# Performance work log

Measured on AMD Instinct MI355X. Metric: run time of the kernel, lower is better.

The kernel has to match this reference:

```python
import jax, jax.numpy as jnp
import numpy as np

B, C, L = 16, 256, 4096
P, Q = 100, 20


def setup_inputs() -> dict:
    key = jax.random.key(0)
    k1, k2, k3, k4 = jax.random.split(key, 4)
    X = jax.random.normal(k1, (B, C, L), dtype=jnp.float32)
    projections = jax.random.normal(k2, (P, C), dtype=jnp.float32)
    # min < max per projection. Projected values ~ N(0, sqrt(C)), so scale ~ sqrt(C).
    scale = jnp.sqrt(jnp.float32(C))
    min_vals = -scale * (1.0 + jax.random.uniform(k3, (P,), dtype=jnp.float32))
    max_vals = scale * (1.0 + jax.random.uniform(k4, (P,), dtype=jnp.float32))
    return {"X": X, "projections": projections, "min_vals": min_vals, "max_vals": max_vals}


def reference(X, projections, min_vals, max_vals):
    # conv1d with kernel size 1 == per-position projection: [B,C,L] x [P,C] -> [B,P,L]
    a = jnp.einsum('bcl,pc->bpl', X, projections)
    # all quantile thresholds at once: thr[p,q] = min + (max-min)*(q+1)/(Q+1)
    fracs = (jnp.arange(1, Q + 1, dtype=jnp.float32)) / jnp.float32(Q + 1)  # [Q]
    thr = min_vals[:, None] + (max_vals - min_vals)[:, None] * fracs[None, :]  # [P,Q]
    # set[b,p,l,q] = a[b,p,l] < thr[p,q]
    set_ = (a[:, :, :, None] < thr[None, :, None, :]).astype(jnp.float32)  # [B,P,L,Q]
    cdf = jnp.mean(set_, axis=2)  # [B,P,Q]
    # transpose(2,1) -> [B,L,P,Q]; reshape -> [B,L,P*Q]; transpose(2,1) -> [B,P*Q,L]
    set_out = jnp.transpose(set_, (0, 2, 1, 3)).reshape(B, L, P * Q)
    set_out = jnp.transpose(set_out, (0, 2, 1))  # [B, P*Q, L]
    cdf_out = cdf.reshape(B, P * Q)
    return (cdf_out, set_out)
```

## Files before the change

kernel.cpp:

```cpp
#include <hip/hip_runtime.h>

#define Bsz 16
#define Cc  256
#define Ll  4096
#define Pp  100
#define Qq  20
#define PQ  (Pp * Qq)

#define LTILE 1024
#define NLT   (Ll / LTILE)
#define GP    10
#define NPG   (Pp / GP)

typedef float f32x4 __attribute__((ext_vector_type(4)));

__global__ __launch_bounds__(256) void csf_main(
    const float* __restrict__ X,
    const float* __restrict__ proj,
    const float* __restrict__ mn,
    const float* __restrict__ mx,
    float* __restrict__ cdf,
    float* __restrict__ set_out) {
    const int lt  = blockIdx.x;
    const int pg  = blockIdx.y;
    const int b   = blockIdx.z;
    const int tid = threadIdx.x;
    const int l0  = lt * LTILE + tid * 4;
    const int p0  = __builtin_amdgcn_readfirstlane(pg * GP);

    const float* Xb = X + (size_t)b * Cc * Ll + l0;

    float acc[GP][4];
#pragma unroll
    for (int i = 0; i < GP; i++)
#pragma unroll
        for (int k = 0; k < 4; k++) acc[i][k] = 0.0f;

#pragma unroll 4
    for (int c = 0; c < Cc; c++) {
        const f32x4 x = *(const f32x4*)(Xb + (size_t)c * Ll);
#pragma unroll
        for (int i = 0; i < GP; i++) {
            const float w = proj[(size_t)(p0 + i) * Cc + c];
            acc[i][0] = __builtin_fmaf(x.x, w, acc[i][0]);
            acc[i][1] = __builtin_fmaf(x.y, w, acc[i][1]);
            acc[i][2] = __builtin_fmaf(x.z, w, acc[i][2]);
            acc[i][3] = __builtin_fmaf(x.w, w, acc[i][3]);
        }
    }

    float fr[Qq];
#pragma unroll
    for (int q = 0; q < Qq; q++) fr[q] = __fdiv_rn((float)(q + 1), 21.0f);

    float* ob = set_out + (size_t)b * PQ * Ll + l0;
    const bool lane0 = ((tid & 63) == 0);

#pragma unroll 1
    for (int i = 0; i < GP; i++) {
        const int p = p0 + i;
        const float mnp = mn[p];
        const float mxp = mx[p];
        const float d = __fsub_rn(mxp, mnp);
#pragma unroll
        for (int q = 0; q < Qq; q++) {
            const float thr = __fadd_rn(mnp, __fmul_rn(d, fr[q]));
            const bool b0 = acc[i][0] < thr;
            const bool b1 = acc[i][1] < thr;
            const bool b2 = acc[i][2] < thr;
            const bool b3 = acc[i][3] < thr;
            f32x4 o;
            o.x = b0 ? 1.0f : 0.0f;
            o.y = b1 ? 1.0f : 0.0f;
            o.z = b2 ? 1.0f : 0.0f;
            o.w = b3 ? 1.0f : 0.0f;
            __builtin_nontemporal_store(o, (f32x4*)(ob + (size_t)(p * Qq + q) * Ll));
            const int cnt = __popcll(__ballot(b0)) + __popcll(__ballot(b1))
                          + __popcll(__ballot(b2)) + __popcll(__ballot(b3));
            if (lane0) {
                atomicAdd(&cdf[(size_t)b * PQ + p * Qq + q],
                          (float)cnt * (1.0f / (float)Ll));
            }
        }
    }
}

extern "C" void kernel_launch(void* const* d_in, const int* in_sizes, int n_in,
                              void* d_out, int out_size, void* d_ws, size_t ws_size,
                              hipStream_t stream) {
    const float* X    = (const float*)d_in[0];
    const float* proj = (const float*)d_in[1];
    const float* mn   = (const float*)d_in[2];
    const float* mx   = (const float*)d_in[3];

    float* cdf     = (float*)d_out;
    float* set_out = cdf + (size_t)Bsz * PQ;

    (void)hipMemsetAsync(cdf, 0, (size_t)Bsz * PQ * sizeof(float), stream);

    dim3 grid(NLT, NPG, Bsz);
    csf_main<<<grid, 256, 0, stream>>>(X, proj, mn, mx, cdf, set_out);
}
```

Measured before the change: 603.1 us.

## Split into projection kernel plus threshold-expansion kernel via workspace buffer

```diff
diff --git a/kernel.cpp b/kernel.cpp
--- a/kernel.cpp
+++ b/kernel.cpp
@@ -7,14 +7,109 @@
 #define Qq  20
 #define PQ  (Pp * Qq)
 
-#define LTILE 1024
-#define NLT   (Ll / LTILE)
-#define GP    10
-#define NPG   (Pp / GP)
-
 typedef float f32x4 __attribute__((ext_vector_type(4)));
 
-__global__ __launch_bounds__(256) void csf_main(
+
+#define K1_PPB 25
+__global__ __launch_bounds__(256) void csf_proj(
+    const float* __restrict__ X,
+    const float* __restrict__ proj,
+    float* __restrict__ a_out) {
+    const int lt = blockIdx.x;
+    const int pg = blockIdx.y;
+    const int b  = blockIdx.z;
+    const int tid  = threadIdx.x;
+    const int wv   = tid >> 6;
+    const int lane = tid & 63;
+    const int l0   = lt * 1024 + wv * 256 + lane * 4;
+    const int p0   = __builtin_amdgcn_readfirstlane(pg * K1_PPB);
+
+    const float* Xb = X + (size_t)b * Cc * Ll + l0;
+    const float* pj = proj + (size_t)p0 * Cc;
+
+    float acc[K1_PPB][4];
+#pragma unroll
+    for (int i = 0; i < K1_PPB; i++)
+#pragma unroll
+        for (int k = 0; k < 4; k++) acc[i][k] = 0.0f;
+
+#pragma unroll 8
+    for (int c = 0; c < Cc; c++) {
+        const f32x4 x = *(const f32x4*)(Xb + (size_t)c * Ll);
+#pragma unroll
+        for (int i = 0; i < K1_PPB; i++) {
+            const float w = pj[(size_t)i * Cc + c];
+            acc[i][0] = __builtin_fmaf(x.x, w, acc[i][0]);
+            acc[i][1] = __builtin_fmaf(x.y, w, acc[i][1]);
+            acc[i][2] = __builtin_fmaf(x.z, w, acc[i][2]);
+            acc[i][3] = __builtin_fmaf(x.w, w, acc[i][3]);
+        }
+    }
+
+    float* ao = a_out + ((size_t)b * Pp + p0) * Ll + l0;
+#pragma unroll
+    for (int i = 0; i < K1_PPB; i++) {
+        f32x4 v;
+        v.x = acc[i][0]; v.y = acc[i][1]; v.z = acc[i][2]; v.w = acc[i][3];
+        *(f32x4*)(ao + (size_t)i * Ll) = v;
+    }
+}
+
+__global__ __launch_bounds__(256) void csf_expand(
+    const float* __restrict__ a_in,
+    const float* __restrict__ mn,
+    const float* __restrict__ mx,
+    float* __restrict__ cdf,
+    float* __restrict__ set_out) {
+    const int p = blockIdx.x;
+    const int b = blockIdx.y;
+    const int tid  = threadIdx.x;
+    const int wv   = tid >> 6;
+    const int lane = tid & 63;
+
+    const float* ar = a_in + ((size_t)b * Pp + p) * Ll + wv * 1024 + lane * 4;
+    f32x4 av[4];
+#pragma unroll
+    for (int k = 0; k < 4; k++) av[k] = *(const f32x4*)(ar + k * 256);
+
+    const float mnp = mn[p];
+    const float mxp = mx[p];
+    const float d = __fsub_rn(mxp, mnp);
+
+    float* ob = set_out + ((size_t)b * PQ + (size_t)p * Qq) * Ll
+              + wv * 1024 + lane * 4;
+    const bool lane0 = (lane == 0);
+
+#pragma unroll 1
+    for (int q = 0; q < Qq; q++) {
+        const float fr  = __fdiv_rn((float)(q + 1), 21.0f);
+        const float thr = __fadd_rn(mnp, __fmul_rn(d, fr));
+        float* orow = ob + (size_t)q * Ll;
+        int cnt = 0;
+#pragma unroll
+        for (int k = 0; k < 4; k++) {
+            const bool b0 = av[k].x < thr;
+            const bool b1 = av[k].y < thr;
+            const bool b2 = av[k].z < thr;
+            const bool b3 = av[k].w < thr;
+            f32x4 o;
+            o.x = b0 ? 1.0f : 0.0f;
+            o.y = b1 ? 1.0f : 0.0f;
+            o.z = b2 ? 1.0f : 0.0f;
+            o.w = b3 ? 1.0f : 0.0f;
+            *(f32x4*)(orow + k * 256) = o;
+            cnt += __popcll(__ballot(b0)) + __popcll(__ballot(b1))
+                 + __popcll(__ballot(b2)) + __popcll(__ballot(b3));
+        }
+        if (lane0) {
+            atomicAdd(&cdf[(size_t)b * PQ + p * Qq + q],
+                      (float)cnt * (1.0f / (float)Ll));
+        }
+    }
+}
+
+#define FGP 10
+__global__ __launch_bounds__(256) void csf_fused(
     const float* __restrict__ X,
     const float* __restrict__ proj,
     const float* __restrict__ mn,
@@ -25,22 +120,20 @@
     const int pg  = blockIdx.y;
     const int b   = blockIdx.z;
     const int tid = threadIdx.x;
-    const int l0  = lt * LTILE + tid * 4;
-    const int p0  = __builtin_amdgcn_readfirstlane(pg * GP);
-
+    const int l0  = lt * 1024 + tid * 4;
+    const int p0  = __builtin_amdgcn_readfirstlane(pg * FGP);
     const float* Xb = X + (size_t)b * Cc * Ll + l0;
 
-    float acc[GP][4];
+    float acc[FGP][4];
 #pragma unroll
-    for (int i = 0; i < GP; i++)
+    for (int i = 0; i < FGP; i++)
 #pragma unroll
         for (int k = 0; k < 4; k++) acc[i][k] = 0.0f;
-
 #pragma unroll 4
     for (int c = 0; c < Cc; c++) {
         const f32x4 x = *(const f32x4*)(Xb + (size_t)c * Ll);
 #pragma unroll
-        for (int i = 0; i < GP; i++) {
+        for (int i = 0; i < FGP; i++) {
             const float w = proj[(size_t)(p0 + i) * Cc + c];
             acc[i][0] = __builtin_fmaf(x.x, w, acc[i][0]);
             acc[i][1] = __builtin_fmaf(x.y, w, acc[i][1]);
@@ -48,19 +141,15 @@
             acc[i][3] = __builtin_fmaf(x.w, w, acc[i][3]);
         }
     }
-
     float fr[Qq];
 #pragma unroll
     for (int q = 0; q < Qq; q++) fr[q] = __fdiv_rn((float)(q + 1), 21.0f);
-
     float* ob = set_out + (size_t)b * PQ * Ll + l0;
     const bool lane0 = ((tid & 63) == 0);
-
 #pragma unroll 1
-    for (int i = 0; i < GP; i++) {
+    for (int i = 0; i < FGP; i++) {
         const int p = p0 + i;
-        const float mnp = mn[p];
-        const float mxp = mx[p];
+        const float mnp = mn[p], mxp = mx[p];
         const float d = __fsub_rn(mxp, mnp);
 #pragma unroll
         for (int q = 0; q < Qq; q++) {
@@ -70,17 +159,14 @@
             const bool b2 = acc[i][2] < thr;
             const bool b3 = acc[i][3] < thr;
             f32x4 o;
-            o.x = b0 ? 1.0f : 0.0f;
-            o.y = b1 ? 1.0f : 0.0f;
-            o.z = b2 ? 1.0f : 0.0f;
-            o.w = b3 ? 1.0f : 0.0f;
+            o.x = b0 ? 1.0f : 0.0f; o.y = b1 ? 1.0f : 0.0f;
+            o.z = b2 ? 1.0f : 0.0f; o.w = b3 ? 1.0f : 0.0f;
             __builtin_nontemporal_store(o, (f32x4*)(ob + (size_t)(p * Qq + q) * Ll));
             const int cnt = __popcll(__ballot(b0)) + __popcll(__ballot(b1))
                           + __popcll(__ballot(b2)) + __popcll(__ballot(b3));
-            if (lane0) {
+            if (lane0)
                 atomicAdd(&cdf[(size_t)b * PQ + p * Qq + q],
                           (float)cnt * (1.0f / (float)Ll));
-            }
         }
     }
 }
@@ -98,6 +184,12 @@
 
     (void)hipMemsetAsync(cdf, 0, (size_t)Bsz * PQ * sizeof(float), stream);
 
-    dim3 grid(NLT, NPG, Bsz);
-    csf_main<<<grid, 256, 0, stream>>>(X, proj, mn, mx, cdf, set_out);
+    const size_t a_bytes = (size_t)Bsz * Pp * Ll * sizeof(float);
+    if (ws_size >= a_bytes) {
+        float* a_buf = (float*)d_ws;
+        csf_proj<<<dim3(4, 4, Bsz), 256, 0, stream>>>(X, proj, a_buf);
+        csf_expand<<<dim3(Pp, Bsz), 256, 0, stream>>>(a_buf, mn, mx, cdf, set_out);
+    } else {
+        csf_fused<<<dim3(4, FGP, Bsz), 256, 0, stream>>>(X, proj, mn, mx, cdf, set_out);
+    }
 }
```

Result: slower. 849.7 us (+40.9%).
